# Performance work log

Measured on AMD Instinct MI355X. Metric: run time of the kernel, lower is better.

## Reference

```python
import jax, jax.numpy as jnp
import numpy as np

N = 50000      # nodes
E = 600000     # edges (avg degree 12)
DIN, DE, DH = 17, 1, 128
L, H, C = 3, 4, 32   # layers, heads, per-head channels (DH = H*C)
NEG_SLOPE = 0.2


def setup_inputs() -> dict:
    key = jax.random.key(0)
    ks = jax.random.split(key, 18)
    rn = lambda k, s, sc: jax.random.normal(k, s, jnp.float32) * sc
    return {
        "x": rn(ks[0], (N, DIN), 1.0),
        "edge_index": jax.random.randint(ks[1], (2, E), 0, N, dtype=jnp.int64),
        "edge_attr": rn(ks[2], (E, DE), 1.0),
        "enc_node_w": rn(ks[3], (DIN, DH), 1.0 / np.sqrt(DIN)),
        "enc_node_b": jnp.zeros((DH,), jnp.float32),
        "enc_edge_w": rn(ks[4], (DE, DH), 1.0),
        "enc_edge_b": jnp.zeros((DH,), jnp.float32),
        "lin_w": rn(ks[5], (L, DH, DH), 1.0 / np.sqrt(DH)),
        "lin_edge_w": rn(ks[6], (L, DH, DH), 1.0 / np.sqrt(DH)),
        "att_src": rn(ks[7], (L, H, C), 1.0 / np.sqrt(C)),
        "att_dst": rn(ks[8], (L, H, C), 1.0 / np.sqrt(C)),
        "att_edge": rn(ks[9], (L, H, C), 1.0 / np.sqrt(C)),
        "gat_bias": jnp.zeros((L, DH), jnp.float32),
        "dec_w1": rn(ks[10], (DH, DH), 1.0 / np.sqrt(DH)),
        "dec_b1": jnp.zeros((DH,), jnp.float32),
        "dec_w2": rn(ks[11], (DH, 2), 1.0 / np.sqrt(DH)),
        "dec_b2": jnp.zeros((2,), jnp.float32),
    }


def _gat_layer(x, src, dst, e_attr, W, We, a_src, a_dst, a_edge, bias):
    """PyG GATConv, concat=True, dropout in eval mode (identity).
    x: [N,DH], src/dst: [E2] (self-loops already appended), e_attr: [E2,DH]."""
    n = x.shape[0]
    h = (x @ W).reshape(n, H, C)                       # [N,H,C]
    alpha_src = jnp.einsum('nhc,hc->nh', h, a_src)     # [N,H]
    alpha_dst = jnp.einsum('nhc,hc->nh', h, a_dst)
    e = (e_attr @ We).reshape(-1, H, C)                # [E2,H,C]
    alpha_e = jnp.einsum('ehc,hc->eh', e, a_edge)      # [E2,H]
    logits = jax.nn.leaky_relu(alpha_src[src] + alpha_dst[dst] + alpha_e, NEG_SLOPE)
    # segment softmax over edges grouped by destination node
    mx = jax.ops.segment_max(logits, dst, num_segments=n)          # [N,H]
    num = jnp.exp(logits - mx[dst])                                # [E2,H]
    den = jax.ops.segment_sum(num, dst, num_segments=n)            # [N,H]
    alpha = num / (den[dst] + 1e-16)                               # [E2,H]
    msg = h[src] * alpha[:, :, None]                               # [E2,H,C]
    out = jax.ops.segment_sum(msg, dst, num_segments=n)            # [N,H,C]
    return out.reshape(n, H * C) + bias


def reference(x, edge_index, edge_attr,
              enc_node_w, enc_node_b, enc_edge_w, enc_edge_b,
              lin_w, lin_edge_w, att_src, att_dst, att_edge, gat_bias,
              dec_w1, dec_b1, dec_w2, dec_b2):
    n = x.shape[0]
    src, dst = edge_index[0], edge_index[1]
    h = x @ enc_node_w + enc_node_b                    # node encoder
    ea = edge_attr @ enc_edge_w + enc_edge_b           # edge encoder [E,DH]
    # add_self_loops with fill_value='mean': self-loop attr = mean of incoming edge attrs
    ea_sum = jax.ops.segment_sum(ea, dst, num_segments=n)
    cnt = jax.ops.segment_sum(jnp.ones((ea.shape[0],), ea.dtype), dst, num_segments=n)
    loop_attr = ea_sum / jnp.maximum(cnt, 1.0)[:, None]
    loop_idx = jnp.arange(n, dtype=src.dtype)
    src_f = jnp.concatenate([src, loop_idx])
    dst_f = jnp.concatenate([dst, loop_idx])
    ea_f = jnp.concatenate([ea, loop_attr], axis=0)    # [E+N,DH]
    for l in range(L):
        h = _gat_layer(h, src_f, dst_f, ea_f,
                       lin_w[l], lin_edge_w[l],
                       att_src[l], att_dst[l], att_edge[l], gat_bias[l])
        h = jax.nn.elu(h)
    h = jax.nn.relu(h @ dec_w1 + dec_b1)
    return h @ dec_w2 + dec_b2                          # [N,2]
```

## Files before the change

kernel.cpp:

```cpp
#include <hip/hip_runtime.h>
#include <hip/hip_fp16.h>
#include <math.h>

#define DIN 17
#define DH  128
#define NH  4
#define CC  32
#define NL  3
#define NEG 0.2f

#define PK_SHIFT 44
#define PK_MASK  ((1ULL << PK_SHIFT) - 1)
#define PK_BIAS  16.0f
#define PK_SCALE 1048576.0f

typedef _Float16 hf;
typedef _Float16 f16x8 __attribute__((ext_vector_type(8)));
typedef float    f32x4 __attribute__((ext_vector_type(4)));

#define NT 9

__global__ void pq_kernel(const float* __restrict__ ew, const float* __restrict__ eb,
                          const float* __restrict__ We, const float* __restrict__ ae,
                          float* __restrict__ pq) {
    int lh = blockIdx.x;
    int l = lh >> 2, h = lh & 3;
    int t = threadIdx.x;
    const float* Wel = We + l * DH * DH;
    const float* ael = ae + l * DH + h * CC;
    float p = 0.f, q = 0.f;
    for (int d = t; d < DH; d += 64) {
        const float* row = Wel + d * DH + h * CC;
        float wp = 0.f;
        for (int c = 0; c < CC; ++c) wp += row[c] * ael[c];
        p += ew[d] * wp;
        q += eb[d] * wp;
    }
    for (int o = 32; o > 0; o >>= 1) { p += __shfl_down(p, o, 64); q += __shfl_down(q, o, 64); }
    if (t == 0) { pq[lh * 2 + 0] = p; pq[lh * 2 + 1] = q; }
}

__global__ void wtprep(const float* __restrict__ lin_w, const float* __restrict__ dec_w1,
                       const float* __restrict__ att_src, const float* __restrict__ att_dst,
                       hf* __restrict__ wfrag) {
    int b = blockIdx.x;
    int m = b / NT, nt = b % NT;
    int lane = threadIdx.x & 63, kk = threadIdx.x >> 6;
    int colr = lane & 15, kg = lane >> 4;
    hf* dst = wfrag + ((((size_t)b * 4 + kk) * 64) + lane) * 8;
    if (nt < 8) {
        const float* src = (m < 3) ? (lin_w + (size_t)m * DH * DH) : dec_w1;
        #pragma unroll
        for (int jj = 0; jj < 8; ++jj) {
            int k = kk * 32 + kg * 8 + jj;
            dst[jj] = (hf)src[k * DH + nt * 16 + colr];
        }
    } else if (m < 3 && colr < 8) {
        int hh = colr >> 1;
        const float* W = lin_w + (size_t)m * DH * DH;
        const float* a = ((colr & 1) ? att_dst : att_src) + m * DH + hh * CC;
        #pragma unroll
        for (int jj = 0; jj < 8; ++jj) {
            int k = kk * 32 + kg * 8 + jj;
            float s = 0.f;
            #pragma unroll
            for (int c = 0; c < CC; ++c) s += W[k * DH + hh * CC + c] * a[c];
            dst[jj] = (hf)s;
        }
    } else {
        #pragma unroll
        for (int jj = 0; jj < 8; ++jj) dst[jj] = (hf)0.f;
    }
}

__global__ void enc_kernel(const float* __restrict__ x, const float* __restrict__ W,
                           const float* __restrict__ b, hf* __restrict__ h16, int N) {
    __shared__ float wl[DIN][DH];
    __shared__ float xs[32][DIN];
    int tid = threadIdx.x;
    int row0 = blockIdx.x * 32;
    for (int i = tid; i < DIN * DH; i += 256) wl[i / DH][i % DH] = W[i];
    for (int i = tid; i < 32 * DIN; i += 256) {
        int r = i / DIN, k = i % DIN;
        int rr = row0 + r; if (rr > N - 1) rr = N - 1;
        xs[r][k] = x[(size_t)rr * DIN + k];
    }
    __syncthreads();
    int c = tid & 127;
    int g = tid >> 7;
    float bias = b[c];
    #pragma unroll
    for (int r = 0; r < 16; ++r) {
        int row = row0 + g * 16 + r;
        if (row >= N) break;
        float acc = bias;
        #pragma unroll
        for (int k = 0; k < DIN; ++k) acc += xs[g * 16 + r][k] * wl[k][c];
        h16[(size_t)row * DH + c] = (hf)acc;
    }
}

#define STAGE_ROWS16(hsrc)                                                        \
    {                                                                             \
        _Pragma("unroll")                                                         \
        for (int i = 0; i < 4; ++i) {                                             \
            int idx = tid + i * 256;           \
            int r = idx >> 4, ch = idx & 15;                                      \
            int gr = row0 + r; if (gr > N - 1) gr = N - 1;                        \
            lds[r * 16 + (ch ^ (r & 7))] =                                        \
                ((const uint4*)((hsrc) + (size_t)gr * DH))[ch];                   \
        }                                                                         \
        __syncthreads();                                                          \
    }

__global__ void __launch_bounds__(256) layer_node(
        const hf* __restrict__ h16, const hf* __restrict__ wfrag,
        __half* __restrict__ h1h, float* __restrict__ as_, float* __restrict__ ad_,
        int N) {
    __shared__ uint4 lds[64 * 16];
    int tid = threadIdx.x;
    int row0 = blockIdx.x * 64;
    STAGE_ROWS16(h16);

    int w = tid >> 6, lane = tid & 63;
    int colr = lane & 15, kg = lane >> 4;
    int lrow = w * 16 + colr;

    f16x8 afr[4];
    #pragma unroll
    for (int kk = 0; kk < 4; ++kk) {
        int ch = (kk * 4 + kg) ^ (colr & 7);
        afr[kk] = *(const f16x8*)&lds[lrow * 16 + ch];
    }

    f32x4 acc[NT];
    #pragma unroll
    for (int nt = 0; nt < NT; ++nt) acc[nt] = (f32x4){0.f, 0.f, 0.f, 0.f};

    const f16x8* wf = (const f16x8*)wfrag;
    #pragma unroll
    for (int nt = 0; nt < NT; ++nt) {
        #pragma unroll
        for (int kk = 0; kk < 4; ++kk) {
            f16x8 bfr = wf[(size_t)(nt * 4 + kk) * 64 + lane];
            acc[nt] = __builtin_amdgcn_mfma_f32_16x16x32_f16(afr[kk], bfr, acc[nt], 0, 0, 0);
        }
    }

    #pragma unroll
    for (int r = 0; r < 4; ++r) {
        int grow = row0 + w * 16 + kg * 4 + r;
        if (grow < N) {
            #pragma unroll
            for (int nt = 0; nt < 8; ++nt)
                h1h[(size_t)grow * DH + nt * 16 + colr] = (__half)(float)acc[nt][r];
        }
    }
    if (colr < 8) {
        int id = colr, hh = id >> 1;
        #pragma unroll
        for (int r = 0; r < 4; ++r) {
            int grow = row0 + w * 16 + kg * 4 + r;
            if (grow < N) {
                float v = (float)acc[8][r];
                if (id & 1) ad_[grow * NH + hh] = v;
                else        as_[grow * NH + hh] = v;
            }
        }
    }
}

__global__ void rank_kernel(const int* __restrict__ ei, const float* __restrict__ ea,
                            unsigned long long* __restrict__ pk, int* __restrict__ rank,
                            int E) {
    int e = blockIdx.x * 256 + threadIdx.x;
    if (e >= E) return;
    int d = ei[E + e];
    unsigned long long enc = (1ULL << PK_SHIFT) |
        (unsigned long long)(int)((ea[e] + PK_BIAS) * PK_SCALE);
    unsigned long long old = atomicAdd(&pk[d], enc);
    rank[e] = (int)(old >> PK_SHIFT);
}

__global__ void scan1(const unsigned long long* __restrict__ pk, int* __restrict__ offs,
                      int* __restrict__ bsum, int N) {
    __shared__ int buf[1024];
    int b = blockIdx.x, t = threadIdx.x, i = b * 1024 + t;
    int v = (i < N) ? (int)(pk[i] >> PK_SHIFT) : 0;
    buf[t] = v;
    __syncthreads();
    int val = v;
    for (int o = 1; o < 1024; o <<= 1) {
        int add = (t >= o) ? buf[t - o] : 0;
        __syncthreads();
        val += add;
        buf[t] = val;
        __syncthreads();
    }
    if (i < N) offs[i] = val - v;
    if (t == 1023) bsum[b] = val;
}

__global__ void scan3(int* __restrict__ offs, const int* __restrict__ bsum,
                      const unsigned long long* __restrict__ pk,
                      int* __restrict__ deg, float* __restrict__ asum, int N) {
    __shared__ int base;
    if (threadIdx.x == 0) {
        int s = 0;
        for (int b = 0; b < (int)blockIdx.x; ++b) s += bsum[b];
        base = s;
    }
    __syncthreads();
    int i = blockIdx.x * 1024 + threadIdx.x;
    if (i >= N) return;
    offs[i] += base;
    unsigned long long p = pk[i];
    int cnt = (int)(p >> PK_SHIFT);
    float s = (float)(p & PK_MASK) * (1.0f / PK_SCALE) - (float)cnt * PK_BIAS;
    deg[i] = cnt;
    asum[i] = s;
}

__global__ void scatter_kernel(const int* __restrict__ ei, const float* __restrict__ ea,
                               const int* __restrict__ offs, const int* __restrict__ rank,
                               int2* __restrict__ csr, int E) {
    int e = blockIdx.x * 256 + threadIdx.x;
    if (e >= E) return;
    int d = ei[E + e];
    int pos = offs[d] + rank[e];
    int2 p; p.x = ei[e]; p.y = __float_as_int(ea[e]);
    csr[pos] = p;
}

__global__ void __launch_bounds__(256) agg_kernel(
        const __half* __restrict__ h1h, const float* __restrict__ as_,
        const float* __restrict__ ad_, const int* __restrict__ offs,
        const int* __restrict__ deg, const float* __restrict__ asum,
        const int2* __restrict__ csr,
        const float* __restrict__ pql, const float* __restrict__ bias,
        hf* __restrict__ hout, int N) {
    int n = blockIdx.x * 4 + (threadIdx.x >> 6);
    if (n >= N) return;
    int lane = threadIdx.x & 63;
    int hd = lane >> 4;
    int c0 = lane * 2;
    int off = offs[n], dg = deg[n];
    float adn = ad_[n * NH + hd];
    float pa = pql[hd * 2 + 0], qa = pql[hd * 2 + 1];

    const __half2* h1v = (const __half2*)h1h;

    float sa = asum[n] / fmaxf((float)dg, 1.f);
    float ael = (dg > 0) ? (sa * pa + qa) : 0.f;
    float l0 = as_[n * NH + hd] + adn + ael;
    l0 = fmaxf(l0, NEG * l0);

    float2 hv = __half22float2(h1v[(size_t)n * 64 + lane]);
    float numS = __expf(l0);
    float denA = numS, a0A = numS * hv.x, a1A = numS * hv.y;
    float denB = 0.f,  a0B = 0.f,         a1B = 0.f;

    int i = 0;
    for (; i + 8 <= dg; i += 8) {
        int2 e[8];
        #pragma unroll
        for (int j = 0; j < 8; ++j) e[j] = csr[off + i + j];
        __half2 q[8];
        #pragma unroll
        for (int j = 0; j < 8; ++j) q[j] = h1v[(size_t)e[j].x * 64 + lane];
        float s[8];
        #pragma unroll
        for (int j = 0; j < 8; ++j) s[j] = as_[e[j].x * NH + hd];
        #pragma unroll
        for (int j = 0; j < 8; ++j) {
            float t = s[j] + adn + __int_as_float(e[j].y) * pa + qa;
            t = fmaxf(t, NEG * t);
            float nm = __expf(t);
            float2 g = __half22float2(q[j]);
            if (j & 1) { denB += nm; a0B = fmaf(nm, g.x, a0B); a1B = fmaf(nm, g.y, a1B); }
            else       { denA += nm; a0A = fmaf(nm, g.x, a0A); a1A = fmaf(nm, g.y, a1A); }
        }
    }
    for (; i + 4 <= dg; i += 4) {
        int2 e[4];
        #pragma unroll
        for (int j = 0; j < 4; ++j) e[j] = csr[off + i + j];
        __half2 q[4];
        #pragma unroll
        for (int j = 0; j < 4; ++j) q[j] = h1v[(size_t)e[j].x * 64 + lane];
        float s[4];
        #pragma unroll
        for (int j = 0; j < 4; ++j) s[j] = as_[e[j].x * NH + hd];
        #pragma unroll
        for (int j = 0; j < 4; ++j) {
            float t = s[j] + adn + __int_as_float(e[j].y) * pa + qa;
            t = fmaxf(t, NEG * t);
            float nm = __expf(t);
            float2 g = __half22float2(q[j]);
            if (j & 1) { denB += nm; a0B = fmaf(nm, g.x, a0B); a1B = fmaf(nm, g.y, a1B); }
            else       { denA += nm; a0A = fmaf(nm, g.x, a0A); a1A = fmaf(nm, g.y, a1A); }
        }
    }
    for (; i < dg; ++i) {
        int2 ep = csr[off + i];
        __half2 qs = h1v[(size_t)ep.x * 64 + lane];
        float lg = as_[ep.x * NH + hd] + adn + __int_as_float(ep.y) * pa + qa;
        lg = fmaxf(lg, NEG * lg);
        float num = __expf(lg);
        float2 gs = __half22float2(qs);
        denA += num;
        a0A = fmaf(num, gs.x, a0A);
        a1A = fmaf(num, gs.y, a1A);
    }
    float den = denA + denB;
    float a0 = a0A + a0B, a1 = a1A + a1B;
    float inv = 1.f / (den + 1e-16f);
    float o0 = a0 * inv + bias[c0];
    float o1 = a1 * inv + bias[c0 + 1];
    o0 = (o0 > 0.f) ? o0 : expm1f(o0);
    o1 = (o1 > 0.f) ? o1 : expm1f(o1);
    union { unsigned int u; hf hx[2]; } st;
    st.hx[0] = (hf)o0; st.hx[1] = (hf)o1;
    ((unsigned int*)hout)[(size_t)n * 64 + lane] = st.u;
}

__global__ void __launch_bounds__(256) dec_kernel(
        const hf* __restrict__ h16, const hf* __restrict__ wfrag,
        const float* __restrict__ b1, const float* __restrict__ w2,
        const float* __restrict__ b2, float* __restrict__ out, int N) {
    __shared__ uint4 lds[64 * 16];
    int tid = threadIdx.x;
    int row0 = blockIdx.x * 64;
    STAGE_ROWS16(h16);

    int w = tid >> 6, lane = tid & 63;
    int colr = lane & 15, kg = lane >> 4;
    int lrow = w * 16 + colr;

    f16x8 afr[4];
    #pragma unroll
    for (int kk = 0; kk < 4; ++kk) {
        int ch = (kk * 4 + kg) ^ (colr & 7);
        afr[kk] = *(const f16x8*)&lds[lrow * 16 + ch];
    }

    f32x4 acc[8];
    #pragma unroll
    for (int nt = 0; nt < 8; ++nt) acc[nt] = (f32x4){0.f, 0.f, 0.f, 0.f};

    const f16x8* wf = (const f16x8*)wfrag;
    #pragma unroll
    for (int nt = 0; nt < 8; ++nt) {
        #pragma unroll
        for (int kk = 0; kk < 4; ++kk) {
            f16x8 bfr = wf[(size_t)(nt * 4 + kk) * 64 + lane];
            acc[nt] = __builtin_amdgcn_mfma_f32_16x16x32_f16(afr[kk], bfr, acc[nt], 0, 0, 0);
        }
    }

    float bb0 = b2[0], bb1 = b2[1];
    float b1v[8], w20[8], w21[8];
    #pragma unroll
    for (int nt = 0; nt < 8; ++nt) {
        int col = nt * 16 + colr;
        b1v[nt] = b1[col];
        w20[nt] = w2[col * 2 + 0];
        w21[nt] = w2[col * 2 + 1];
    }
    #pragma unroll
    for (int r = 0; r < 4; ++r) {
        float p0 = 0.f, p1 = 0.f;
        #pragma unroll
        for (int nt = 0; nt < 8; ++nt) {
            float hid = fmaxf((float)acc[nt][r] + b1v[nt], 0.f);
            p0 = fmaf(hid, w20[nt], p0);
            p1 = fmaf(hid, w21[nt], p1);
        }
        #pragma unroll
        for (int o = 1; o < 16; o <<= 1) {
            p0 += __shfl_xor(p0, o, 16);
            p1 += __shfl_xor(p1, o, 16);
        }
        int grow = row0 + w * 16 + kg * 4 + r;
        if (colr == 0 && grow < N) {
            out[grow * 2 + 0] = p0 + bb0;
            out[grow * 2 + 1] = p1 + bb1;
        }
    }
}

extern "C" void kernel_launch(void* const* d_in, const int* in_sizes, int n_in,
                              void* d_out, int out_size, void* d_ws, size_t ws_size,
                              hipStream_t stream) {
    const float* x          = (const float*)d_in[0];
    const int*   ei         = (const int*)d_in[1];
    const float* eattr      = (const float*)d_in[2];
    const float* enc_node_w = (const float*)d_in[3];
    const float* enc_node_b = (const float*)d_in[4];
    const float* enc_edge_w = (const float*)d_in[5];
    const float* enc_edge_b = (const float*)d_in[6];
    const float* lin_w      = (const float*)d_in[7];
    const float* lin_edge_w = (const float*)d_in[8];
    const float* att_src    = (const float*)d_in[9];
    const float* att_dst    = (const float*)d_in[10];
    const float* att_edge   = (const float*)d_in[11];
    const float* gat_bias   = (const float*)d_in[12];
    const float* dec_w1     = (const float*)d_in[13];
    const float* dec_b1     = (const float*)d_in[14];
    const float* dec_w2     = (const float*)d_in[15];
    const float* dec_b2     = (const float*)d_in[16];

    const int E = in_sizes[2];
    const int N = in_sizes[0] / DIN;

    char* w = (char*)d_ws;
    auto alloc = [&](size_t bytes) -> void* {
        void* p = (void*)w;
        w += (bytes + 511) & ~((size_t)511);
        return p;
    };
    hf*     h16   = (hf*)alloc((size_t)N * DH * 2);
    __half* h1h   = (__half*)alloc((size_t)N * DH * 2);
    float* as_    = (float*)alloc((size_t)N * NH * 4);
    float* ad_    = (float*)alloc((size_t)N * NH * 4);
    unsigned long long* pk = (unsigned long long*)alloc((size_t)N * 8);
    int*   rank   = (int*)alloc((size_t)E * 4);
    int*   deg    = (int*)alloc((size_t)N * 4);
    float* asum   = (float*)alloc((size_t)N * 4);
    int*   offs   = (int*)alloc((size_t)N * 4);
    int*   bsum   = (int*)alloc(64 * 4);
    int2*  csr    = (int2*)alloc((size_t)E * 8);
    float* pq     = (float*)alloc(NL * NH * 2 * 4);
    hf*    wfrag  = (hf*)alloc((size_t)4 * NT * 4 * 64 * 8 * 2);

    hipMemsetAsync(pk, 0, (size_t)N * 8, stream);

    pq_kernel<<<NL * NH, 64, 0, stream>>>(enc_edge_w, enc_edge_b, lin_edge_w, att_edge, pq);
    wtprep<<<4 * NT, 256, 0, stream>>>(lin_w, dec_w1, att_src, att_dst, wfrag);
    enc_kernel<<<(N + 31) / 32, 256, 0, stream>>>(x, enc_node_w, enc_node_b, h16, N);
    rank_kernel<<<(E + 255) / 256, 256, 0, stream>>>(ei, eattr, pk, rank, E);

    int nb = (N + 1023) / 1024;
    scan1<<<nb, 1024, 0, stream>>>(pk, offs, bsum, N);
    scan3<<<nb, 1024, 0, stream>>>(offs, bsum, pk, deg, asum, N);
    scatter_kernel<<<(E + 255) / 256, 256, 0, stream>>>(ei, eattr, offs, rank, csr, E);

    const size_t mstride = (size_t)NT * 4 * 64 * 8;
    for (int l = 0; l < NL; ++l) {
        layer_node<<<(N + 63) / 64, 256, 0, stream>>>(h16, wfrag + (size_t)l * mstride,
                                                      h1h, as_, ad_, N);
        agg_kernel<<<(N + 3) / 4, 256, 0, stream>>>(h1h, as_, ad_, offs, deg, asum, csr,
                                                    pq + l * NH * 2, gat_bias + l * DH, h16, N);
    }
    dec_kernel<<<(N + 63) / 64, 256, 0, stream>>>(h16, wfrag + (size_t)3 * mstride,
                                                  dec_b1, dec_w2, dec_b2,
                                                  (float*)d_out, N);
}
```

Measured before the change: 327.0 us.

## Fuse setup kernels and replace two-pass scan with atomic-cursor offset allocation

Merges the memset, pq and weight-prep kernels into one prep kernel, and fuses edge ranking with the node encoder into one launch. The two-pass block scan is replaced by per-wavefront prefix sums that claim a base offset via an atomic cursor. That pass is fused with the first layer's node transform. Degree and self-loop attribute sums are now decoded from the packed counter inside the aggregation kernel, which drops the deg and asum arrays. The aim is to cut launch count and serial scan overhead. In exchange, CSR segment placement is no longer in node order, which may reduce memory locality in aggregation.

New measurement: 322.4 us. About the same (-1.4%).

```diff
diff --git a/kernel.cpp b/kernel.cpp
--- a/kernel.cpp
+++ b/kernel.cpp
@@ -20,107 +20,125 @@
 
 #define NT 9
 
-__global__ void pq_kernel(const float* __restrict__ ew, const float* __restrict__ eb,
-                          const float* __restrict__ We, const float* __restrict__ ae,
-                          float* __restrict__ pq) {
-    int lh = blockIdx.x;
-    int l = lh >> 2, h = lh & 3;
-    int t = threadIdx.x;
-    const float* Wel = We + l * DH * DH;
-    const float* ael = ae + l * DH + h * CC;
-    float p = 0.f, q = 0.f;
-    for (int d = t; d < DH; d += 64) {
-        const float* row = Wel + d * DH + h * CC;
-        float wp = 0.f;
-        for (int c = 0; c < CC; ++c) wp += row[c] * ael[c];
-        p += ew[d] * wp;
-        q += eb[d] * wp;
-    }
-    for (int o = 32; o > 0; o >>= 1) { p += __shfl_down(p, o, 64); q += __shfl_down(q, o, 64); }
-    if (t == 0) { pq[lh * 2 + 0] = p; pq[lh * 2 + 1] = q; }
-}
-
-__global__ void wtprep(const float* __restrict__ lin_w, const float* __restrict__ dec_w1,
-                       const float* __restrict__ att_src, const float* __restrict__ att_dst,
-                       hf* __restrict__ wfrag) {
-    int b = blockIdx.x;
-    int m = b / NT, nt = b % NT;
-    int lane = threadIdx.x & 63, kk = threadIdx.x >> 6;
-    int colr = lane & 15, kg = lane >> 4;
-    hf* dst = wfrag + ((((size_t)b * 4 + kk) * 64) + lane) * 8;
-    if (nt < 8) {
-        const float* src = (m < 3) ? (lin_w + (size_t)m * DH * DH) : dec_w1;
-        #pragma unroll
-        for (int jj = 0; jj < 8; ++jj) {
-            int k = kk * 32 + kg * 8 + jj;
-            dst[jj] = (hf)src[k * DH + nt * 16 + colr];
-        }
-    } else if (m < 3 && colr < 8) {
-        int hh = colr >> 1;
-        const float* W = lin_w + (size_t)m * DH * DH;
-        const float* a = ((colr & 1) ? att_dst : att_src) + m * DH + hh * CC;
-        #pragma unroll
-        for (int jj = 0; jj < 8; ++jj) {
-            int k = kk * 32 + kg * 8 + jj;
-            float s = 0.f;
+__global__ void __launch_bounds__(256) prep_kernel(
+        const float* __restrict__ ew, const float* __restrict__ eb,
+        const float* __restrict__ We, const float* __restrict__ ae,
+        const float* __restrict__ lin_w, const float* __restrict__ dec_w1,
+        const float* __restrict__ att_src, const float* __restrict__ att_dst,
+        float* __restrict__ pq, hf* __restrict__ wfrag,
+        unsigned long long* __restrict__ pk, int* __restrict__ cursor, int N) {
+    int b = blockIdx.x, tid = threadIdx.x;
+    if (b < 12) {
+        if (tid < 64) {
+            int l = b >> 2, h = b & 3;
+            const float* Wel = We + l * DH * DH;
+            const float* ael = ae + l * DH + h * CC;
+            float p = 0.f, q = 0.f;
+            for (int d = tid; d < DH; d += 64) {
+                const float* row = Wel + d * DH + h * CC;
+                float wp = 0.f;
+                for (int c = 0; c < CC; ++c) wp += row[c] * ael[c];
+                p += ew[d] * wp;
+                q += eb[d] * wp;
+            }
+            for (int o = 32; o > 0; o >>= 1) {
+                p += __shfl_down(p, o, 64);
+                q += __shfl_down(q, o, 64);
+            }
+            if (tid == 0) { pq[b * 2 + 0] = p; pq[b * 2 + 1] = q; }
+        }
+    } else if (b < 48) {
+        int bb = b - 12;
+        int m = bb / NT, nt = bb % NT;
+        int lane = tid & 63, kk = tid >> 6;
+        int colr = lane & 15, kg = lane >> 4;
+        hf* dst = wfrag + ((((size_t)bb * 4 + kk) * 64) + lane) * 8;
+        if (nt < 8) {
+            const float* src = (m < 3) ? (lin_w + (size_t)m * DH * DH) : dec_w1;
             #pragma unroll
-            for (int c = 0; c < CC; ++c) s += W[k * DH + hh * CC + c] * a[c];
-            dst[jj] = (hf)s;
+            for (int jj = 0; jj < 8; ++jj) {
+                int k = kk * 32 + kg * 8 + jj;
+                dst[jj] = (hf)src[k * DH + nt * 16 + colr];
+            }
+        } else if (m < 3 && colr < 8) {
+            int hh = colr >> 1;
+            const float* W = lin_w + (size_t)m * DH * DH;
+            const float* a = ((colr & 1) ? att_dst : att_src) + m * DH + hh * CC;
+            #pragma unroll
+            for (int jj = 0; jj < 8; ++jj) {
+                int k = kk * 32 + kg * 8 + jj;
+                float s = 0.f;
+                #pragma unroll
+                for (int c = 0; c < CC; ++c) s += W[k * DH + hh * CC + c] * a[c];
+                dst[jj] = (hf)s;
+            }
+        } else {
+            #pragma unroll
+            for (int jj = 0; jj < 8; ++jj) dst[jj] = (hf)0.f;
         }
     } else {
-        #pragma unroll
-        for (int jj = 0; jj < 8; ++jj) dst[jj] = (hf)0.f;
-    }
-}
-
-__global__ void enc_kernel(const float* __restrict__ x, const float* __restrict__ W,
-                           const float* __restrict__ b, hf* __restrict__ h16, int N) {
+        int i = (b - 48) * 256 + tid;
+        if (i < N) pk[i] = 0ULL;
+        if (b == 48 && tid == 0) cursor[0] = 0;
+    }
+}
+
+__global__ void __launch_bounds__(256) rank_enc_kernel(
+        const int* __restrict__ ei, const float* __restrict__ ea,
+        unsigned long long* __restrict__ pk, int* __restrict__ rank,
+        const float* __restrict__ x, const float* __restrict__ Wn,
+        const float* __restrict__ bn, hf* __restrict__ h16,
+        int E, int N, int EB) {
     __shared__ float wl[DIN][DH];
     __shared__ float xs[32][DIN];
     int tid = threadIdx.x;
-    int row0 = blockIdx.x * 32;
-    for (int i = tid; i < DIN * DH; i += 256) wl[i / DH][i % DH] = W[i];
-    for (int i = tid; i < 32 * DIN; i += 256) {
-        int r = i / DIN, k = i % DIN;
-        int rr = row0 + r; if (rr > N - 1) rr = N - 1;
-        xs[r][k] = x[(size_t)rr * DIN + k];
-    }
-    __syncthreads();
-    int c = tid & 127;
-    int g = tid >> 7;
-    float bias = b[c];
-    #pragma unroll
-    for (int r = 0; r < 16; ++r) {
-        int row = row0 + g * 16 + r;
-        if (row >= N) break;
-        float acc = bias;
-        #pragma unroll
-        for (int k = 0; k < DIN; ++k) acc += xs[g * 16 + r][k] * wl[k][c];
-        h16[(size_t)row * DH + c] = (hf)acc;
-    }
-}
-
-#define STAGE_ROWS16(hsrc)                                                        \
-    {                                                                             \
-        _Pragma("unroll")                                                         \
-        for (int i = 0; i < 4; ++i) {                                             \
-            int idx = tid + i * 256;           \
-            int r = idx >> 4, ch = idx & 15;                                      \
-            int gr = row0 + r; if (gr > N - 1) gr = N - 1;                        \
-            lds[r * 16 + (ch ^ (r & 7))] =                                        \
-                ((const uint4*)((hsrc) + (size_t)gr * DH))[ch];                   \
-        }                                                                         \
-        __syncthreads();                                                          \
-    }
-
-__global__ void __launch_bounds__(256) layer_node(
+    if ((int)blockIdx.x < EB) {
+        int e = blockIdx.x * 256 + tid;
+        if (e >= E) return;
+        int d = ei[E + e];
+        unsigned long long enc = (1ULL << PK_SHIFT) |
+            (unsigned long long)(int)((ea[e] + PK_BIAS) * PK_SCALE);
+        unsigned long long old = atomicAdd(&pk[d], enc);
+        rank[e] = (int)(old >> PK_SHIFT);
+    } else {
+        int row0 = (blockIdx.x - EB) * 32;
+        for (int i = tid; i < DIN * DH; i += 256) wl[i / DH][i % DH] = Wn[i];
+        for (int i = tid; i < 32 * DIN; i += 256) {
+            int r = i / DIN, k = i % DIN;
+            int rr = row0 + r; if (rr > N - 1) rr = N - 1;
+            xs[r][k] = x[(size_t)rr * DIN + k];
+        }
+        __syncthreads();
+        int c = tid & 127;
+        int g = tid >> 7;
+        float bias = bn[c];
+        #pragma unroll
+        for (int r = 0; r < 16; ++r) {
+            int row = row0 + g * 16 + r;
+            if (row >= N) break;
+            float acc = bias;
+            #pragma unroll
+            for (int k = 0; k < DIN; ++k) acc += xs[g * 16 + r][k] * wl[k][c];
+            h16[(size_t)row * DH + c] = (hf)acc;
+        }
+    }
+}
+
+__device__ __forceinline__ void ln_body(
         const hf* __restrict__ h16, const hf* __restrict__ wfrag,
         __half* __restrict__ h1h, float* __restrict__ as_, float* __restrict__ ad_,
-        int N) {
+        int N, int blk) {
     __shared__ uint4 lds[64 * 16];
     int tid = threadIdx.x;
-    int row0 = blockIdx.x * 64;
-    STAGE_ROWS16(h16);
+    int row0 = blk * 64;
+    #pragma unroll
+    for (int i = 0; i < 4; ++i) {
+        int idx = tid + i * 256;
+        int r = idx >> 4, ch = idx & 15;
+        int gr = row0 + r; if (gr > N - 1) gr = N - 1;
+        lds[r * 16 + (ch ^ (r & 7))] = ((const uint4*)(h16 + (size_t)gr * DH))[ch];
+    }
+    __syncthreads();
 
     int w = tid >> 6, lane = tid & 63;
     int colr = lane & 15, kg = lane >> 4;
@@ -170,55 +188,37 @@
     }
 }
 
-__global__ void rank_kernel(const int* __restrict__ ei, const float* __restrict__ ea,
-                            unsigned long long* __restrict__ pk, int* __restrict__ rank,
-                            int E) {
-    int e = blockIdx.x * 256 + threadIdx.x;
-    if (e >= E) return;
-    int d = ei[E + e];
-    unsigned long long enc = (1ULL << PK_SHIFT) |
-        (unsigned long long)(int)((ea[e] + PK_BIAS) * PK_SCALE);
-    unsigned long long old = atomicAdd(&pk[d], enc);
-    rank[e] = (int)(old >> PK_SHIFT);
-}
-
-__global__ void scan1(const unsigned long long* __restrict__ pk, int* __restrict__ offs,
-                      int* __restrict__ bsum, int N) {
-    __shared__ int buf[1024];
-    int b = blockIdx.x, t = threadIdx.x, i = b * 1024 + t;
-    int v = (i < N) ? (int)(pk[i] >> PK_SHIFT) : 0;
-    buf[t] = v;
-    __syncthreads();
-    int val = v;
-    for (int o = 1; o < 1024; o <<= 1) {
-        int add = (t >= o) ? buf[t - o] : 0;
-        __syncthreads();
-        val += add;
-        buf[t] = val;
-        __syncthreads();
-    }
-    if (i < N) offs[i] = val - v;
-    if (t == 1023) bsum[b] = val;
-}
-
-__global__ void scan3(int* __restrict__ offs, const int* __restrict__ bsum,
-                      const unsigned long long* __restrict__ pk,
-                      int* __restrict__ deg, float* __restrict__ asum, int N) {
-    __shared__ int base;
-    if (threadIdx.x == 0) {
-        int s = 0;
-        for (int b = 0; b < (int)blockIdx.x; ++b) s += bsum[b];
-        base = s;
-    }
-    __syncthreads();
-    int i = blockIdx.x * 1024 + threadIdx.x;
-    if (i >= N) return;
-    offs[i] += base;
-    unsigned long long p = pk[i];
-    int cnt = (int)(p >> PK_SHIFT);
-    float s = (float)(p & PK_MASK) * (1.0f / PK_SCALE) - (float)cnt * PK_BIAS;
-    deg[i] = cnt;
-    asum[i] = s;
+__global__ void __launch_bounds__(256) alloc_ln_kernel(
+        const unsigned long long* __restrict__ pk, int* __restrict__ offs,
+        int* __restrict__ cursor,
+        const hf* __restrict__ h16, const hf* __restrict__ wfrag,
+        __half* __restrict__ h1h, float* __restrict__ as_, float* __restrict__ ad_,
+        int N, int AB) {
+    if ((int)blockIdx.x < AB) {
+        int i = blockIdx.x * 256 + threadIdx.x;
+        int lane = threadIdx.x & 63;
+        int d = (i < N) ? (int)(pk[i] >> PK_SHIFT) : 0;
+        int incl = d;
+        #pragma unroll
+        for (int o = 1; o < 64; o <<= 1) {
+            int v = __shfl_up(incl, o, 64);
+            if (lane >= o) incl += v;
+        }
+        int total = __shfl(incl, 63, 64);
+        int base = 0;
+        if (lane == 0) base = atomicAdd(cursor, total);
+        base = __shfl(base, 0, 64);
+        if (i < N) offs[i] = base + incl - d;
+    } else {
+        ln_body(h16, wfrag, h1h, as_, ad_, N, blockIdx.x - AB);
+    }
+}
+
+__global__ void __launch_bounds__(256) layer_node(
+        const hf* __restrict__ h16, const hf* __restrict__ wfrag,
+        __half* __restrict__ h1h, float* __restrict__ as_, float* __restrict__ ad_,
+        int N) {
+    ln_body(h16, wfrag, h1h, as_, ad_, N, blockIdx.x);
 }
 
 __global__ void scatter_kernel(const int* __restrict__ ei, const float* __restrict__ ea,
@@ -235,7 +235,7 @@
 __global__ void __launch_bounds__(256) agg_kernel(
         const __half* __restrict__ h1h, const float* __restrict__ as_,
         const float* __restrict__ ad_, const int* __restrict__ offs,
-        const int* __restrict__ deg, const float* __restrict__ asum,
+        const unsigned long long* __restrict__ pkbuf,
         const int2* __restrict__ csr,
         const float* __restrict__ pql, const float* __restrict__ bias,
         hf* __restrict__ hout, int N) {
@@ -244,13 +244,16 @@
     int lane = threadIdx.x & 63;
     int hd = lane >> 4;
     int c0 = lane * 2;
-    int off = offs[n], dg = deg[n];
+    int off = offs[n];
+    unsigned long long p = pkbuf[n];
+    int dg = (int)(p >> PK_SHIFT);
+    float asumv = (float)(p & PK_MASK) * (1.0f / PK_SCALE) - (float)dg * PK_BIAS;
     float adn = ad_[n * NH + hd];
     float pa = pql[hd * 2 + 0], qa = pql[hd * 2 + 1];
 
     const __half2* h1v = (const __half2*)h1h;
 
-    float sa = asum[n] / fmaxf((float)dg, 1.f);
+    float sa = asumv / fmaxf((float)dg, 1.f);
     float ael = (dg > 0) ? (sa * pa + qa) : 0.f;
     float l0 = as_[n * NH + hd] + adn + ael;
     l0 = fmaxf(l0, NEG * l0);
@@ -331,7 +334,14 @@
     __shared__ uint4 lds[64 * 16];
     int tid = threadIdx.x;
     int row0 = blockIdx.x * 64;
-    STAGE_ROWS16(h16);
+    #pragma unroll
+    for (int i = 0; i < 4; ++i) {
+        int idx = tid + i * 256;
+        int r = idx >> 4, ch = idx & 15;
+        int gr = row0 + r; if (gr > N - 1) gr = N - 1;
+        lds[r * 16 + (ch ^ (r & 7))] = ((const uint4*)(h16 + (size_t)gr * DH))[ch];
+    }
+    __syncthreads();
 
     int w = tid >> 6, lane = tid & 63;
     int colr = lane & 15, kg = lane >> 4;
@@ -425,34 +435,38 @@
     float* ad_    = (float*)alloc((size_t)N * NH * 4);
     unsigned long long* pk = (unsigned long long*)alloc((size_t)N * 8);
     int*   rank   = (int*)alloc((size_t)E * 4);
-    int*   deg    = (int*)alloc((size_t)N * 4);
-    float* asum   = (float*)alloc((size_t)N * 4);
     int*   offs   = (int*)alloc((size_t)N * 4);
-    int*   bsum   = (int*)alloc(64 * 4);
+    int*   cursor = (int*)alloc(64);
     int2*  csr    = (int2*)alloc((size_t)E * 8);
     float* pq     = (float*)alloc(NL * NH * 2 * 4);
     hf*    wfrag  = (hf*)alloc((size_t)4 * NT * 4 * 64 * 8 * 2);
 
-    hipMemsetAsync(pk, 0, (size_t)N * 8, stream);
-
-    pq_kernel<<<NL * NH, 64, 0, stream>>>(enc_edge_w, enc_edge_b, lin_edge_w, att_edge, pq);
-    wtprep<<<4 * NT, 256, 0, stream>>>(lin_w, dec_w1, att_src, att_dst, wfrag);
-    enc_kernel<<<(N + 31) / 32, 256, 0, stream>>>(x, enc_node_w, enc_node_b, h16, N);
-    rank_kernel<<<(E + 255) / 256, 256, 0, stream>>>(ei, eattr, pk, rank, E);
-
-    int nb = (N + 1023) / 1024;
-    scan1<<<nb, 1024, 0, stream>>>(pk, offs, bsum, N);
-    scan3<<<nb, 1024, 0, stream>>>(offs, bsum, pk, deg, asum, N);
-    scatter_kernel<<<(E + 255) / 256, 256, 0, stream>>>(ei, eattr, offs, rank, csr, E);
-
+    const int EB   = (E + 255) / 256;
+    const int NB32 = (N + 31) / 32;
+    const int AB   = (N + 255) / 256;
+    const int LNB  = (N + 63) / 64;
     const size_t mstride = (size_t)NT * 4 * 64 * 8;
-    for (int l = 0; l < NL; ++l) {
-        layer_node<<<(N + 63) / 64, 256, 0, stream>>>(h16, wfrag + (size_t)l * mstride,
-                                                      h1h, as_, ad_, N);
-        agg_kernel<<<(N + 3) / 4, 256, 0, stream>>>(h1h, as_, ad_, offs, deg, asum, csr,
+
+    prep_kernel<<<48 + AB, 256, 0, stream>>>(enc_edge_w, enc_edge_b, lin_edge_w, att_edge,
+                                             lin_w, dec_w1, att_src, att_dst,
+                                             pq, wfrag, pk, cursor, N);
+    rank_enc_kernel<<<EB + NB32, 256, 0, stream>>>(ei, eattr, pk, rank,
+                                                   x, enc_node_w, enc_node_b, h16,
+                                                   E, N, EB);
+    alloc_ln_kernel<<<AB + LNB, 256, 0, stream>>>(pk, offs, cursor,
+                                                  h16, wfrag + 0 * mstride,
+                                                  h1h, as_, ad_, N, AB);
+    scatter_kernel<<<EB, 256, 0, stream>>>(ei, eattr, offs, rank, csr, E);
+
+    agg_kernel<<<(N + 3) / 4, 256, 0, stream>>>(h1h, as_, ad_, offs, pk, csr,
+                                                pq + 0 * NH * 2, gat_bias + 0 * DH, h16, N);
+    for (int l = 1; l < NL; ++l) {
+        layer_node<<<LNB, 256, 0, stream>>>(h16, wfrag + (size_t)l * mstride,
+                                            h1h, as_, ad_, N);
+        agg_kernel<<<(N + 3) / 4, 256, 0, stream>>>(h1h, as_, ad_, offs, pk, csr,
                                                     pq + l * NH * 2, gat_bias + l * DH, h16, N);
     }
-    dec_kernel<<<(N + 63) / 64, 256, 0, stream>>>(h16, wfrag + (size_t)3 * mstride,
-                                                  dec_b1, dec_w2, dec_b2,
-                                                  (float*)d_out, N);
-}
+    dec_kernel<<<LNB, 256, 0, stream>>>(h16, wfrag + (size_t)3 * mstride,
+                                        dec_b1, dec_w2, dec_b2,
+                                        (float*)d_out, N);
+}
```
